# Kernel tuning notes

Hardware: AMD Instinct MI355X
Metric: run time of the kernel (lower is better)

The kernel has to match this reference:

```python
import jax, jax.numpy as jnp
import numpy as np

H = 128        # hidden_channels
R = 32         # num_rbf
L = 2          # num_layers
CUTOFF = 4.5   # cutoff_upper (cutoff_lower = 0)
N_ATOMS = 2048
N_EDGES = 32768


def _tensor_norm(t):
    # Frobenius norm squared over the trailing 3x3 -> [N, H]
    return jnp.sum(t * t, axis=(-2, -1))


def _decompose(t):
    # Split into isotropic (I), antisymmetric (A), traceless symmetric (S) parts.
    eye = jnp.eye(3, dtype=t.dtype)
    I = (jnp.trace(t, axis1=-2, axis2=-1) / 3.0)[..., None, None] * eye
    A = 0.5 * (t - jnp.swapaxes(t, -2, -1))
    S = 0.5 * (t + jnp.swapaxes(t, -2, -1)) - I
    return I, A, S


def _chan_mix(T, W):
    # torch nn.Linear(H, H, bias=False) applied on the channel axis of [N,H,3,3]
    return jnp.einsum('nhij,gh->ngij', T, W)


def _interaction(X, edge_index, edge_weight, edge_attr, q,
                 W1, b1, W2, b2, W3, b3, Wt):
    N = X.shape[0]
    src, dst = edge_index[0], edge_index[1]
    # cosine cutoff (cutoff_lower = 0)
    C = 0.5 * (jnp.cos(edge_weight * (jnp.pi / CUTOFF)) + 1.0)
    C = C * (edge_weight < CUTOFF).astype(C.dtype)
    # edge scalar MLP: R -> H -> 2H -> 3H, silu
    ea = jax.nn.silu(edge_attr @ W1.T + b1)
    ea = jax.nn.silu(ea @ W2.T + b2)
    ea = jax.nn.silu(ea @ W3.T + b3)
    ea = (ea * C[:, None]).reshape(-1, H, 3)       # [E, H, 3]
    # normalize node tensors
    X = X / (_tensor_norm(X) + 1.0)[..., None, None]
    I, A, S = _decompose(X)
    I = _chan_mix(I, Wt[0])
    A = _chan_mix(A, Wt[1])
    S = _chan_mix(S, Wt[2])
    Y = I + A + S
    # per-edge tensor messages (Im + Am + Sm fused before the scatter)
    msg = (ea[:, :, 0, None, None] * I[dst]
           + ea[:, :, 1, None, None] * A[dst]
           + ea[:, :, 2, None, None] * S[dst])   # [E, H, 3, 3]
    M = jax.ops.segment_sum(msg, src, num_segments=N)
    # O(3) group: symmetrized tensor product, scaled by charge factor
    AB = jnp.matmul(M, Y) + jnp.matmul(Y, M)
    I, A, S = _decompose((1.0 + 0.1 * q[:, None, None, None]) * AB)
    normp1 = (_tensor_norm(I + A + S) + 1.0)[..., None, None]
    I, A, S = I / normp1, A / normp1, S / normp1
    I = _chan_mix(I, Wt[3])
    A = _chan_mix(A, Wt[4])
    S = _chan_mix(S, Wt[5])
    dX = I + A + S
    return X + dX + (1.0 + 0.1 * q[:, None, None, None]) * jnp.matmul(dX, dX)


def setup_inputs() -> dict:
    key = jax.random.key(0)
    ks = jax.random.split(key, 10)
    N, E = N_ATOMS, N_EDGES
    X = jax.random.normal(ks[0], (N, H, 3, 3), jnp.float32)
    edge_index = jax.random.randint(ks[1], (2, E), 0, N, jnp.int32)
    edge_weight = jax.random.uniform(ks[2], (E,), jnp.float32, 0.1, CUTOFF)
    edge_attr = jax.random.normal(ks[3], (E, R), jnp.float32)
    q = jax.random.normal(ks[4], (N,), jnp.float32) * 0.1
    s = 0.05
    Ws1 = jax.random.normal(ks[5], (L, H, R), jnp.float32) * s
    bs1 = jnp.zeros((L, H), jnp.float32)
    Ws2 = jax.random.normal(ks[6], (L, 2 * H, H), jnp.float32) * s
    bs2 = jnp.zeros((L, 2 * H), jnp.float32)
    Ws3 = jax.random.normal(ks[7], (L, 3 * H, 2 * H), jnp.float32) * s
    bs3 = jnp.zeros((L, 3 * H), jnp.float32)
    Wt = jax.random.normal(ks[8], (L, 6, H, H), jnp.float32) * s
    return dict(X=X, edge_attr=edge_attr, edge_weight=edge_weight, q=q,
                Ws1=Ws1, bs1=bs1, Ws2=Ws2, bs2=bs2, Ws3=Ws3, bs3=bs3,
                Wt=Wt, edge_index=edge_index)


def reference(X, edge_attr, edge_weight, q, Ws1, bs1, Ws2, bs2, Ws3, bs3, Wt, edge_index):
    for l in range(L):
        X = _interaction(X, edge_index, edge_weight, edge_attr, q,
                         Ws1[l], bs1[l], Ws2[l], bs2[l], Ws3[l], bs3[l], Wt[l])
    return X
```

## Files before the change

kernel.cpp:

```cpp
#include <hip/hip_runtime.h>
#include <hip/hip_bf16.h>
#include <math.h>

#define H 128
#define R 32
#define NATOMS 2048
#define NEDGES 32768
#define NH (NATOMS * H)
#define NP 1152
#define CUTOFF_F 4.5f
#define PI_OVER_CUTOFF 0.6981317007977318f

typedef __bf16 bf16x8 __attribute__((ext_vector_type(8)));
typedef float f32x4 __attribute__((ext_vector_type(4)));
typedef short short8 __attribute__((ext_vector_type(8)));

__device__ __forceinline__ float silu_f(float x) {
    return x / (1.f + __expf(-x));
}
__device__ __forceinline__ float b2f(unsigned short u) {
    return __uint_as_float(((unsigned)u) << 16);
}
__device__ __forceinline__ unsigned short f2b(float f) {
    __hip_bfloat16 h = __float2bfloat16(f);
    return __builtin_bit_cast(unsigned short, h);
}

__device__ __forceinline__ void build_full(const float d[9], float m[9]) {
    float i0 = d[0], a01 = d[1], a02 = d[2], a12 = d[3];
    float s00 = d[4], s01 = d[5], s02 = d[6], s11 = d[7], s12 = d[8];
    float s22 = -(s00 + s11);
    m[0] = i0 + s00;  m[1] = a01 + s01;  m[2] = a02 + s02;
    m[3] = s01 - a01; m[4] = i0 + s11;   m[5] = a12 + s12;
    m[6] = s02 - a02; m[7] = s12 - a12;  m[8] = i0 + s22;
}

#define C0 (NEDGES * R)
#define C1 (2 * H * R)
#define C2 (2 * 2 * H * H)
#define C3 (2 * 3 * H * 2 * H)
#define C4 (2 * 6 * H * H)
#define CAST_TOTAL (C0 + C1 + C2 + C3 + C4 + 2048)
__global__ __launch_bounds__(256) void k_cast_all(
        const float* __restrict__ ea, const float* __restrict__ w1,
        const float* __restrict__ w2, const float* __restrict__ w3,
        const float* __restrict__ wt,
        __hip_bfloat16* __restrict__ oea, __hip_bfloat16* __restrict__ ow1,
        __hip_bfloat16* __restrict__ ow2, __hip_bfloat16* __restrict__ ow3,
        __hip_bfloat16* __restrict__ owt, int* __restrict__ cnt) {
    int i = blockIdx.x * 256 + threadIdx.x;
    if (i < C0) { oea[i] = __float2bfloat16(ea[i]); return; }
    i -= C0;
    if (i < C1) { ow1[i] = __float2bfloat16(w1[i]); return; }
    i -= C1;
    if (i < C2) { ow2[i] = __float2bfloat16(w2[i]); return; }
    i -= C2;
    if (i < C3) { ow3[i] = __float2bfloat16(w3[i]); return; }
    i -= C3;
    if (i < C4) { owt[i] = __float2bfloat16(wt[i]); return; }
    i -= C4;
    if (i < 2048) cnt[i] = 0;
}

__global__ __launch_bounds__(256) void k_node_prep(
        const float* __restrict__ X, float* __restrict__ Xn,
        __hip_bfloat16* __restrict__ Db) {
    int i = blockIdx.x * 256 + threadIdx.x;
    if (i >= NH) return;
    const float* x = X + (size_t)i * 9;
    float v[9];
    float ss = 0.f;
#pragma unroll
    for (int j = 0; j < 9; j++) { v[j] = x[j]; ss += v[j] * v[j]; }
    float inv = 1.f / (ss + 1.f);
#pragma unroll
    for (int j = 0; j < 9; j++) { v[j] *= inv; Xn[(size_t)i * 9 + j] = v[j]; }
    float i0 = (v[0] + v[4] + v[8]) * (1.f / 3.f);
    unsigned short* D = (unsigned short*)Db + (size_t)(i >> 7) * NP + (i & 127);
    D[0 * H] = f2b(i0);
    D[1 * H] = f2b(0.5f * (v[1] - v[3]));
    D[2 * H] = f2b(0.5f * (v[2] - v[6]));
    D[3 * H] = f2b(0.5f * (v[5] - v[7]));
    D[4 * H] = f2b(v[0] - i0);
    D[5 * H] = f2b(0.5f * (v[1] + v[3]));
    D[6 * H] = f2b(0.5f * (v[2] + v[6]));
    D[7 * H] = f2b(v[4] - i0);
    D[8 * H] = f2b(0.5f * (v[5] + v[7]));
}

struct TGm {
    static constexpr int BKm = 64;
    static constexpr int RB  = 128;
    static constexpr int SWZ = 7;
    static constexpr int NIT = 2;
    static constexpr int ABYTES = 128 * RB;
    static constexpr int BBYTES = 64 * RB;
    static constexpr int AISS = ABYTES / 4096;
    static constexpr int BISS = BBYTES / 4096;
    static constexpr int LDSB = ABYTES + BBYTES;
};

__device__ __forceinline__ void tile_gemm_mix(
        const __hip_bfloat16* __restrict__ A, int strideA,
        const __hip_bfloat16* __restrict__ W,
        int m0, int n0, char* lds, f32x4 acc[4][2]) {
    using T = TGm;
    const int t = threadIdx.x;
    const int lane = t & 63;
    const int w = t >> 6;

    auto stage = [&](int b, int it) {
        const int k0 = it * T::BKm;
        char* As = lds + b * T::LDSB;
        char* Bs = As + T::ABYTES;
#pragma unroll
        for (int i = 0; i < T::AISS; i++) {
            int base = (w * T::AISS + i) * 1024;
            int lin = base + lane * 16;
            int row = lin / T::RB;
            int slot = (lin % T::RB) >> 4;
            int sl = slot ^ (row & T::SWZ);
            const char* src = (const char*)(A + (size_t)(m0 + row) * strideA + k0) + sl * 16;
            __builtin_amdgcn_global_load_lds(
                (const __attribute__((address_space(1))) void*)src,
                (__attribute__((address_space(3))) void*)(As + base), 16, 0, 0);
        }
#pragma unroll
        for (int i = 0; i < T::BISS; i++) {
            int base = (w * T::BISS + i) * 1024;
            int lin = base + lane * 16;
            int row = lin / T::RB;
            int slot = (lin % T::RB) >> 4;
            int sl = slot ^ (row & T::SWZ);
            const char* src = (const char*)(W + (size_t)(n0 + row) * H + k0) + sl * 16;
            __builtin_amdgcn_global_load_lds(
                (const __attribute__((address_space(1))) void*)src,
                (__attribute__((address_space(3))) void*)(Bs + base), 16, 0, 0);
        }
    };

    auto compute = [&](int b) {
        const char* As = lds + b * T::LDSB;
        const char* Bs = As + T::ABYTES;
        const int wm = (w & 1) * 64;
        const int wn = (w >> 1) * 32;
        const int rA = wm + (lane & 15);
        const int rB = wn + (lane & 15);
        const int c = lane >> 4;
#pragma unroll
        for (int kk = 0; kk < T::BKm / 32; kk++) {
            bf16x8 av[4], bv[2];
#pragma unroll
            for (int mf = 0; mf < 4; mf++) {
                int row = rA + mf * 16;
                int sp = (kk * 4 + c) ^ (row & T::SWZ);
                av[mf] = __builtin_bit_cast(bf16x8,
                    *(const short8*)(As + row * T::RB + sp * 16));
            }
#pragma unroll
            for (int nf = 0; nf < 2; nf++) {
                int row = rB + nf * 16;
                int sp = (kk * 4 + c) ^ (row & T::SWZ);
                bv[nf] = __builtin_bit_cast(bf16x8,
                    *(const short8*)(Bs + row * T::RB + sp * 16));
            }
#pragma unroll
            for (int mf = 0; mf < 4; mf++)
#pragma unroll
                for (int nf = 0; nf < 2; nf++)
                    acc[mf][nf] = __builtin_amdgcn_mfma_f32_16x16x32_bf16(
                        av[mf], bv[nf], acc[mf][nf], 0, 0, 0);
        }
    };

    stage(0, 0);
    asm volatile("s_waitcnt vmcnt(0)" ::: "memory");
    __syncthreads();
    for (int it = 0; it < T::NIT; it++) {
        int b = it & 1;
        if (it + 1 < T::NIT) stage(b ^ 1, it + 1);
        compute(b);
        asm volatile("s_waitcnt vmcnt(0)" ::: "memory");
        __syncthreads();
    }
}

__global__ __launch_bounds__(256) void k_mix(
        const __hip_bfloat16* __restrict__ Db, const __hip_bfloat16* __restrict__ Wtb,
        __hip_bfloat16* __restrict__ Outp, int partOff) {
    __shared__ char lds[2 * TGm::LDSB];
    int c = blockIdx.z;
    int part = (c == 0) ? 0 : ((c < 4) ? 1 : 2);
    const __hip_bfloat16* A = Db + (size_t)c * H;
    const __hip_bfloat16* W = Wtb + (size_t)(partOff + part) * H * H;
    unsigned short* Out = (unsigned short*)Outp + (size_t)c * H;
    const int lane = threadIdx.x & 63;
    const int w = threadIdx.x >> 6;
    const int wm = (w & 1) * 64, wn = (w >> 1) * 32;
    const int m0 = blockIdx.x * 128, n0 = blockIdx.y * 64;
    f32x4 acc[4][2] = {};
    tile_gemm_mix(A, NP, W, m0, n0, lds, acc);
#pragma unroll
    for (int mf = 0; mf < 4; mf++)
#pragma unroll
        for (int r = 0; r < 4; r++) {
            int row = m0 + wm + mf * 16 + (lane >> 4) * 4 + r;
#pragma unroll
            for (int nf = 0; nf < 2; nf++) {
                int col = n0 + wn + nf * 16 + (lane & 15);
                Out[(size_t)row * NP + col] = f2b(acc[mf][nf][r]);
            }
        }
}

#define ETILE 64
#define PAD0 40
#define PAD1 136
#define PAD2 264
#define SA2_B (ETILE * PAD2 * 2)
#define SA1_B (ETILE * PAD1 * 2)
#define SEA_OFF SA1_B

__global__ __launch_bounds__(512, 4) void k_mlp_fused(
        const __hip_bfloat16* __restrict__ eaB,
        const __hip_bfloat16* __restrict__ W1b, const __hip_bfloat16* __restrict__ W2b,
        const __hip_bfloat16* __restrict__ W3b,
        const float* __restrict__ bs1, const float* __restrict__ bs2,
        const float* __restrict__ bs3, const float* __restrict__ ew,
        __hip_bfloat16* __restrict__ ea3g) {
    const int l = blockIdx.z;
    const unsigned short* W1 = (const unsigned short*)W1b + (size_t)l * (H * R);
    const unsigned short* W2 = (const unsigned short*)W2b + (size_t)l * (2 * H * H);
    const unsigned short* W3 = (const unsigned short*)W3b + (size_t)l * (3 * H * 2 * H);
    const float* b1 = bs1 + (size_t)l * H;
    const float* b2 = bs2 + (size_t)l * 2 * H;
    const float* b3 = bs3 + (size_t)l * 3 * H;
    unsigned short* outp = (unsigned short*)ea3g + (size_t)l * NEDGES * 384;
    const int e0 = blockIdx.x * ETILE;

    __shared__ char smem[SA2_B + ETILE * 4 + 16];
    unsigned short* sA2 = (unsigned short*)smem;
    unsigned short* sA1 = (unsigned short*)smem;
    unsigned short* sEA = (unsigned short*)(smem + SEA_OFF);
    float* sEW = (float*)(smem + SA2_B);

    const int t = threadIdx.x;
    const int lane = t & 63;
    const int w = t >> 6;
    const int q = lane >> 4;
    const int li = lane & 15;

    {
        if (t < 256) {
            int row = t >> 2, c8 = t & 3;
            *(uint4*)(sEA + row * PAD0 + c8 * 8) =
                *(const uint4*)((const unsigned short*)eaB + (size_t)(e0 + row) * R + c8 * 8);
        }
        if (t < ETILE) sEW[t] = ew[e0 + t];
    }
    __syncthreads();

    {
        f32x4 acc1[4] = {};
        const int col = w * 16 + li;
        bf16x8 bv = __builtin_bit_cast(bf16x8,
            *(const short8*)(W1 + (size_t)col * R + q * 8));
#pragma unroll
        for (int mf = 0; mf < 4; mf++) {
            int row = mf * 16 + li;
            bf16x8 av = __builtin_bit_cast(bf16x8,
                *(const short8*)(sEA + row * PAD0 + q * 8));
            acc1[mf] = __builtin_amdgcn_mfma_f32_16x16x32_bf16(
                av, bv, acc1[mf], 0, 0, 0);
        }
        float bb = b1[col];
#pragma unroll
        for (int mf = 0; mf < 4; mf++)
#pragma unroll
            for (int r = 0; r < 4; r++) {
                int row = mf * 16 + q * 4 + r;
                sA1[row * PAD1 + col] = f2b(silu_f(acc1[mf][r] + bb));
            }
    }
    __syncthreads();

    {
        f32x4 acc2[4][2] = {};
        bf16x8 b2v[2][2];
#pragma unroll
        for (int nf = 0; nf < 2; nf++)
            b2v[0][nf] = __builtin_bit_cast(bf16x8,
                *(const short8*)(W2 + (size_t)(w * 32 + nf * 16 + li) * H + q * 8));
#pragma unroll
        for (int ks = 0; ks < 4; ks++) {
            const int cur = ks & 1;
            if (ks < 3) {
#pragma unroll
                for (int nf = 0; nf < 2; nf++)
                    b2v[cur ^ 1][nf] = __builtin_bit_cast(bf16x8,
                        *(const short8*)(W2 + (size_t)(w * 32 + nf * 16 + li) * H
                                         + (ks + 1) * 32 + q * 8));
            }
            bf16x8 av[4];
#pragma unroll
            for (int mf = 0; mf < 4; mf++)
                av[mf] = __builtin_bit_cast(bf16x8,
                    *(const short8*)(sA1 + (mf * 16 + li) * PAD1 + ks * 32 + q * 8));
            __builtin_amdgcn_s_setprio(1);
#pragma unroll
            for (int mf = 0; mf < 4; mf++)
#pragma unroll
                for (int nf = 0; nf < 2; nf++)
                    acc2[mf][nf] = __builtin_amdgcn_mfma_f32_16x16x32_bf16(
                        av[mf], b2v[cur][nf], acc2[mf][nf], 0, 0, 0);
            __builtin_amdgcn_s_setprio(0);
        }
        float bb[2];
#pragma unroll
        for (int nf = 0; nf < 2; nf++) bb[nf] = b2[w * 32 + nf * 16 + li];
        __syncthreads();
#pragma unroll
        for (int mf = 0; mf < 4; mf++)
#pragma unroll
            for (int r = 0; r < 4; r++) {
                int row = mf * 16 + q * 4 + r;
#pragma unroll
                for (int nf = 0; nf < 2; nf++) {
                    int col = w * 32 + nf * 16 + li;
                    sA2[row * PAD2 + col] = f2b(silu_f(acc2[mf][nf][r] + bb[nf]));
                }
            }
    }
    __syncthreads();

#pragma unroll
    for (int hn = 0; hn < 2; hn++) {
        const int NF = (hn == 0) ? 2 : 1;
        const int cbase = w * 48 + hn * 32;
        f32x4 acc3[4][2] = {};
        bf16x8 b3v[2][2];
#pragma unroll
        for (int nf = 0; nf < 2; nf++)
            if (nf < NF)
                b3v[0][nf] = __builtin_bit_cast(bf16x8,
                    *(const short8*)(W3 + (size_t)(cbase + nf * 16 + li) * (2 * H) + q * 8));
#pragma unroll
        for (int ks = 0; ks < 8; ks++) {
            const int cur = ks & 1;
            if (ks < 7) {
#pragma unroll
                for (int nf = 0; nf < 2; nf++)
                    if (nf < NF)
                        b3v[cur ^ 1][nf] = __builtin_bit_cast(bf16x8,
                            *(const short8*)(W3 + (size_t)(cbase + nf * 16 + li) * (2 * H)
                                             + (ks + 1) * 32 + q * 8));
            }
            bf16x8 av[4];
#pragma unroll
            for (int mf = 0; mf < 4; mf++)
                av[mf] = __builtin_bit_cast(bf16x8,
                    *(const short8*)(sA2 + (mf * 16 + li) * PAD2 + ks * 32 + q * 8));
            __builtin_amdgcn_s_setprio(1);
#pragma unroll
            for (int mf = 0; mf < 4; mf++)
#pragma unroll
                for (int nf = 0; nf < 2; nf++)
                    if (nf < NF)
                        acc3[mf][nf] = __builtin_amdgcn_mfma_f32_16x16x32_bf16(
                            av[mf], b3v[cur][nf], acc3[mf][nf], 0, 0, 0);
            __builtin_amdgcn_s_setprio(0);
        }
        float bb[2];
#pragma unroll
        for (int nf = 0; nf < 2; nf++)
            bb[nf] = (nf < NF) ? b3[cbase + nf * 16 + li] : 0.f;
#pragma unroll
        for (int mf = 0; mf < 4; mf++)
#pragma unroll
            for (int r = 0; r < 4; r++) {
                int row = mf * 16 + q * 4 + r;
                float wv = sEW[row];
                float cs = (wv < CUTOFF_F) ? 0.5f * (__cosf(wv * PI_OVER_CUTOFF) + 1.f) : 0.f;
#pragma unroll
                for (int nf = 0; nf < 2; nf++)
                    if (nf < NF) {
                        int col = cbase + nf * 16 + li;
                        float x = silu_f(acc3[mf][nf][r] + bb[nf]) * cs;
                        outp[(size_t)(e0 + row) * 384 + col] = f2b(x);
                    }
            }
    }
}

__global__ __launch_bounds__(256) void k_hist(
        const int* __restrict__ eidx, int* __restrict__ cnt) {
    int e = blockIdx.x * 256 + threadIdx.x;
    if (e < NEDGES) atomicAdd(&cnt[eidx[e]], 1);
}

__global__ __launch_bounds__(256) void k_scan(
        const int* __restrict__ cnt, int* __restrict__ rowstart,
        int* __restrict__ cursor) {
    __shared__ int partial[256];
    int t = threadIdx.x;
    int loc[8];
    int run = 0;
#pragma unroll
    for (int j = 0; j < 8; j++) {
        int v = cnt[t * 8 + j];
        loc[j] = run; run += v;
    }
    partial[t] = run;
    __syncthreads();
    if (t == 0) {
        int acc = 0;
        for (int i = 0; i < 256; i++) { int v = partial[i]; partial[i] = acc; acc += v; }
        rowstart[2048] = acc;
    }
    __syncthreads();
    int base = partial[t];
#pragma unroll
    for (int j = 0; j < 8; j++) {
        rowstart[t * 8 + j] = base + loc[j];
        cursor[t * 8 + j] = base + loc[j];
    }
}

__global__ __launch_bounds__(256) void k_fill(
        const int* __restrict__ eidx, int* __restrict__ cursor,
        int* __restrict__ elist) {
    int e = blockIdx.x * 256 + threadIdx.x;
    if (e >= NEDGES) return;
    int src = eidx[e];
    int pos = atomicAdd(&cursor[src], 1);
    elist[pos] = e;
}

__global__ __launch_bounds__(256) void k_gather_ab(
        const __hip_bfloat16* __restrict__ ea ,
        const int* __restrict__ eidx,
        const int* __restrict__ rowstart, const int* __restrict__ elist,
        const __hip_bfloat16* __restrict__ Yb, const float* __restrict__ q,
        __hip_bfloat16* __restrict__ Tb) {
    int gid = blockIdx.x * 256 + threadIdx.x;
    int n = gid >> 7;
    int t7 = gid & 127;
    int hp = t7 >> 1;
    int half = t7 & 1;
    int h0 = hp << 1;
    int beg = rowstart[n], end = rowstart[n + 1];
    const unsigned short* Y = (const unsigned short*)Yb;
    float acc[9][2];
#pragma unroll
    for (int c = 0; c < 9; c++) { acc[c][0] = 0.f; acc[c][1] = 0.f; }
    for (int idx = beg + half; idx < end; idx += 2) {
        int e = elist[idx];
        int dst = eidx[NEDGES + e];
        const unsigned short* eap = (const unsigned short*)ea + (size_t)e * 384 + h0 * 3;
        unsigned u0 = *(const unsigned*)(eap);
        unsigned u1 = *(const unsigned*)(eap + 2);
        unsigned u2 = *(const unsigned*)(eap + 4);
        float w0a = b2f(u0 & 0xffff), w1a = b2f(u0 >> 16);
        float w2a = b2f(u1 & 0xffff), w0b = b2f(u1 >> 16);
        float w1b = b2f(u2 & 0xffff), w2b = b2f(u2 >> 16);
        const unsigned short* yp = Y + (size_t)dst * NP + h0;
        ushort2 y;
        y = *(const ushort2*)(yp + 0 * H); acc[0][0] += w0a * b2f(y.x); acc[0][1] += w0b * b2f(y.y);
        y = *(const ushort2*)(yp + 1 * H); acc[1][0] += w1a * b2f(y.x); acc[1][1] += w1b * b2f(y.y);
        y = *(const ushort2*)(yp + 2 * H); acc[2][0] += w1a * b2f(y.x); acc[2][1] += w1b * b2f(y.y);
        y = *(const ushort2*)(yp + 3 * H); acc[3][0] += w1a * b2f(y.x); acc[3][1] += w1b * b2f(y.y);
#pragma unroll
        for (int c = 4; c < 9; c++) {
            y = *(const ushort2*)(yp + c * H);
            acc[c][0] += w2a * b2f(y.x); acc[c][1] += w2b * b2f(y.y);
        }
    }
#pragma unroll
    for (int c = 0; c < 9; c++) {
        acc[c][0] += __shfl_xor(acc[c][0], 1);
        acc[c][1] += __shfl_xor(acc[c][1], 1);
    }
    int hcol = h0 + half;
    const unsigned short* yp = Y + (size_t)n * NP + hcol;
    float scale = 1.f + 0.1f * q[n];
    float md[9], yd[9];
#pragma unroll
    for (int c = 0; c < 9; c++) {
        md[c] = acc[c][half];
        yd[c] = b2f(yp[(size_t)c * H]);
    }
    float m[9], yf[9];
    build_full(md, m);
    build_full(yd, yf);
    float ab[9];
#pragma unroll
    for (int ii = 0; ii < 3; ii++)
#pragma unroll
        for (int jj = 0; jj < 3; jj++) {
            float s = 0.f;
#pragma unroll
            for (int kk = 0; kk < 3; kk++)
                s += m[ii * 3 + kk] * yf[kk * 3 + jj] + yf[ii * 3 + kk] * m[kk * 3 + jj];
            ab[ii * 3 + jj] = s;
        }
    float nrm = 0.f;
#pragma unroll
    for (int j = 0; j < 9; j++) { ab[j] *= scale; nrm += ab[j] * ab[j]; }
    float inv = 1.f / (nrm + 1.f);
    float tr3 = (ab[0] + ab[4] + ab[8]) * (1.f / 3.f);
    unsigned short* T = (unsigned short*)Tb + (size_t)n * NP + hcol;
    T[0 * H] = f2b(tr3 * inv);
    T[1 * H] = f2b(0.5f * (ab[1] - ab[3]) * inv);
    T[2 * H] = f2b(0.5f * (ab[2] - ab[6]) * inv);
    T[3 * H] = f2b(0.5f * (ab[5] - ab[7]) * inv);
    T[4 * H] = f2b((ab[0] - tr3) * inv);
    T[5 * H] = f2b(0.5f * (ab[1] + ab[3]) * inv);
    T[6 * H] = f2b(0.5f * (ab[2] + ab[6]) * inv);
    T[7 * H] = f2b((ab[4] - tr3) * inv);
    T[8 * H] = f2b(0.5f * (ab[5] + ab[7]) * inv);
}

template <bool PREP>
__global__ __launch_bounds__(256) void k_final(
        const __hip_bfloat16* __restrict__ dXb, const float* __restrict__ Xn,
        const float* __restrict__ q, float* __restrict__ Xout,
        float* __restrict__ XnW, __hip_bfloat16* __restrict__ Db) {
    int i = blockIdx.x * 256 + threadIdx.x;
    if (i >= NH) return;
    const unsigned short* dX = (const unsigned short*)dXb + (size_t)(i >> 7) * NP + (i & 127);
    float dd[9];
#pragma unroll
    for (int c = 0; c < 9; c++) dd[c] = b2f(dX[(size_t)c * H]);
    float dx[9];
    build_full(dd, dx);
    float scale = 1.f + 0.1f * q[i >> 7];
    float out[9];
#pragma unroll
    for (int ii = 0; ii < 3; ii++)
#pragma unroll
        for (int jj = 0; jj < 3; jj++) {
            float s = 0.f;
#pragma unroll
            for (int kk = 0; kk < 3; kk++)
                s += dx[ii * 3 + kk] * dx[kk * 3 + jj];
            out[ii * 3 + jj] = Xn[(size_t)i * 9 + ii * 3 + jj] + dx[ii * 3 + jj] + scale * s;
        }
#pragma unroll
    for (int j = 0; j < 9; j++) Xout[(size_t)i * 9 + j] = out[j];
    if (PREP) {
        float ss = 0.f;
#pragma unroll
        for (int j = 0; j < 9; j++) ss += out[j] * out[j];
        float inv = 1.f / (ss + 1.f);
        float v[9];
#pragma unroll
        for (int j = 0; j < 9; j++) { v[j] = out[j] * inv; XnW[(size_t)i * 9 + j] = v[j]; }
        float i0 = (v[0] + v[4] + v[8]) * (1.f / 3.f);
        unsigned short* D = (unsigned short*)Db + (size_t)(i >> 7) * NP + (i & 127);
        D[0 * H] = f2b(i0);
        D[1 * H] = f2b(0.5f * (v[1] - v[3]));
        D[2 * H] = f2b(0.5f * (v[2] - v[6]));
        D[3 * H] = f2b(0.5f * (v[5] - v[7]));
        D[4 * H] = f2b(v[0] - i0);
        D[5 * H] = f2b(0.5f * (v[1] + v[3]));
        D[6 * H] = f2b(0.5f * (v[2] + v[6]));
        D[7 * H] = f2b(v[4] - i0);
        D[8 * H] = f2b(0.5f * (v[5] + v[7]));
    }
}

extern "C" void kernel_launch(void* const* d_in, const int* in_sizes, int n_in,
                              void* d_out, int out_size, void* d_ws, size_t ws_size,
                              hipStream_t stream) {
    const float* X          = (const float*)d_in[0];
    const float* edge_attr  = (const float*)d_in[1];
    const float* edge_weight= (const float*)d_in[2];
    const float* q          = (const float*)d_in[3];
    const float* Ws1        = (const float*)d_in[4];
    const float* bs1        = (const float*)d_in[5];
    const float* Ws2        = (const float*)d_in[6];
    const float* bs2        = (const float*)d_in[7];
    const float* Ws3        = (const float*)d_in[8];
    const float* bs3        = (const float*)d_in[9];
    const float* Wt         = (const float*)d_in[10];
    const int*   eidx       = (const int*)d_in[11];
    float* Xout = (float*)d_out;

    char* p = (char*)d_ws;
    auto alloc = [&](size_t bytes) -> char* {
        char* r = p; p += (bytes + 255) & ~(size_t)255; return r;
    };
    size_t nodeBytes = (size_t)NH * 9 * sizeof(float);
    float* Xn   = (float*)alloc(nodeBytes);
    __hip_bfloat16* Db = (__hip_bfloat16*)alloc((size_t)NH * 9 * 2);
    __hip_bfloat16* Yb = (__hip_bfloat16*)alloc((size_t)NH * 9 * 2);
    __hip_bfloat16* eaB = (__hip_bfloat16*)alloc((size_t)C0 * 2);
    __hip_bfloat16* W1b = (__hip_bfloat16*)alloc((size_t)C1 * 2);
    __hip_bfloat16* W2b = (__hip_bfloat16*)alloc((size_t)C2 * 2);
    __hip_bfloat16* W3b = (__hip_bfloat16*)alloc((size_t)C3 * 2);
    __hip_bfloat16* Wtb = (__hip_bfloat16*)alloc((size_t)C4 * 2);
    __hip_bfloat16* ea3g = (__hip_bfloat16*)alloc((size_t)2 * NEDGES * 384 * 2);
    int* cnt      = (int*)alloc(2048 * 4);
    int* rowstart = (int*)alloc(2049 * 4);
    int* cursor   = (int*)alloc(2048 * 4);
    int* elist    = (int*)alloc(NEDGES * 4);

    k_cast_all<<<(CAST_TOTAL + 255) / 256, 256, 0, stream>>>(
        edge_attr, Ws1, Ws2, Ws3, Wt, eaB, W1b, W2b, W3b, Wtb, cnt);

    k_hist<<<NEDGES / 256, 256, 0, stream>>>(eidx, cnt);
    k_scan<<<1, 256, 0, stream>>>(cnt, rowstart, cursor);
    k_fill<<<NEDGES / 256, 256, 0, stream>>>(eidx, cursor, elist);

    k_node_prep<<<NH / 256, 256, 0, stream>>>(X, Xn, Db);

    k_mlp_fused<<<dim3(NEDGES / ETILE, 1, 2), 512, 0, stream>>>(
        eaB, W1b, W2b, W3b, bs1, bs2, bs3, edge_weight, ea3g);

    for (int l = 0; l < 2; l++) {
        const __hip_bfloat16* Wtl = Wtb + (size_t)l * 6 * H * H;
        const __hip_bfloat16* ea3 = ea3g + (size_t)l * NEDGES * 384;

        k_mix<<<dim3(NATOMS / 128, 2, 9), 256, 0, stream>>>(Db, Wtl, Yb, 0);
        k_gather_ab<<<NH / 256, 256, 0, stream>>>(
            ea3, eidx, rowstart, elist, Yb, q, Db);
        k_mix<<<dim3(NATOMS / 128, 2, 9), 256, 0, stream>>>(Db, Wtl, Yb, 3);
        if (l == 0)
            k_final<true><<<NH / 256, 256, 0, stream>>>(Yb, Xn, q, Xout, Xn, Db);
        else
            k_final<false><<<NH / 256, 256, 0, stream>>>(Yb, Xn, q, Xout, nullptr, nullptr);
    }
}
```

Baseline: 161.5 us.

## Transpose edge-MLP MFMA operands for vectorized stores and fold node prep into cast

The edge MLP GEMMs swap operand roles so weights become the A operand and edge activations the B operand. Each lane then holds four consecutive output channels and can write them as one 8-byte vector to LDS and global memory instead of scalar bf16 stores. The third layer is also restructured from two column halves into a single 3x4 fragment pass, and biases are loaded as float4. Separately, the node normalization and decomposition is merged into the cast kernel to remove one launch, at the cost of more registers in the third GEMM and a larger combined kernel.

Result: no change. 163.5 us (+1.3%).

```diff
diff --git a/kernel.cpp b/kernel.cpp
--- a/kernel.cpp
+++ b/kernel.cpp
@@ -14,6 +14,7 @@
 typedef __bf16 bf16x8 __attribute__((ext_vector_type(8)));
 typedef float f32x4 __attribute__((ext_vector_type(4)));
 typedef short short8 __attribute__((ext_vector_type(8)));
+typedef unsigned short u16x4 __attribute__((ext_vector_type(4)));
 
 __device__ __forceinline__ float silu_f(float x) {
     return x / (1.f + __expf(-x));
@@ -40,14 +41,17 @@
 #define C2 (2 * 2 * H * H)
 #define C3 (2 * 3 * H * 2 * H)
 #define C4 (2 * 6 * H * H)
-#define CAST_TOTAL (C0 + C1 + C2 + C3 + C4 + 2048)
+#define C5 2048
+#define CAST_TOTAL (C0 + C1 + C2 + C3 + C4 + C5 + NH)
 __global__ __launch_bounds__(256) void k_cast_all(
         const float* __restrict__ ea, const float* __restrict__ w1,
         const float* __restrict__ w2, const float* __restrict__ w3,
         const float* __restrict__ wt,
         __hip_bfloat16* __restrict__ oea, __hip_bfloat16* __restrict__ ow1,
         __hip_bfloat16* __restrict__ ow2, __hip_bfloat16* __restrict__ ow3,
-        __hip_bfloat16* __restrict__ owt, int* __restrict__ cnt) {
+        __hip_bfloat16* __restrict__ owt, int* __restrict__ cnt,
+        const float* __restrict__ X, float* __restrict__ Xn,
+        __hip_bfloat16* __restrict__ Db) {
     int i = blockIdx.x * 256 + threadIdx.x;
     if (i < C0) { oea[i] = __float2bfloat16(ea[i]); return; }
     i -= C0;
@@ -59,33 +63,29 @@
     i -= C3;
     if (i < C4) { owt[i] = __float2bfloat16(wt[i]); return; }
     i -= C4;
-    if (i < 2048) cnt[i] = 0;
-}
-
-__global__ __launch_bounds__(256) void k_node_prep(
-        const float* __restrict__ X, float* __restrict__ Xn,
-        __hip_bfloat16* __restrict__ Db) {
-    int i = blockIdx.x * 256 + threadIdx.x;
-    if (i >= NH) return;
-    const float* x = X + (size_t)i * 9;
-    float v[9];
-    float ss = 0.f;
-#pragma unroll
-    for (int j = 0; j < 9; j++) { v[j] = x[j]; ss += v[j] * v[j]; }
-    float inv = 1.f / (ss + 1.f);
-#pragma unroll
-    for (int j = 0; j < 9; j++) { v[j] *= inv; Xn[(size_t)i * 9 + j] = v[j]; }
-    float i0 = (v[0] + v[4] + v[8]) * (1.f / 3.f);
-    unsigned short* D = (unsigned short*)Db + (size_t)(i >> 7) * NP + (i & 127);
-    D[0 * H] = f2b(i0);
-    D[1 * H] = f2b(0.5f * (v[1] - v[3]));
-    D[2 * H] = f2b(0.5f * (v[2] - v[6]));
-    D[3 * H] = f2b(0.5f * (v[5] - v[7]));
-    D[4 * H] = f2b(v[0] - i0);
-    D[5 * H] = f2b(0.5f * (v[1] + v[3]));
-    D[6 * H] = f2b(0.5f * (v[2] + v[6]));
-    D[7 * H] = f2b(v[4] - i0);
-    D[8 * H] = f2b(0.5f * (v[5] + v[7]));
+    if (i < C5) { cnt[i] = 0; return; }
+    i -= C5;
+    if (i < NH) {
+        const float* x = X + (size_t)i * 9;
+        float v[9];
+        float ss = 0.f;
+#pragma unroll
+        for (int j = 0; j < 9; j++) { v[j] = x[j]; ss += v[j] * v[j]; }
+        float inv = 1.f / (ss + 1.f);
+#pragma unroll
+        for (int j = 0; j < 9; j++) { v[j] *= inv; Xn[(size_t)i * 9 + j] = v[j]; }
+        float i0 = (v[0] + v[4] + v[8]) * (1.f / 3.f);
+        unsigned short* D = (unsigned short*)Db + (size_t)(i >> 7) * NP + (i & 127);
+        D[0 * H] = f2b(i0);
+        D[1 * H] = f2b(0.5f * (v[1] - v[3]));
+        D[2 * H] = f2b(0.5f * (v[2] - v[6]));
+        D[3 * H] = f2b(0.5f * (v[5] - v[7]));
+        D[4 * H] = f2b(v[0] - i0);
+        D[5 * H] = f2b(0.5f * (v[1] + v[3]));
+        D[6 * H] = f2b(0.5f * (v[2] + v[6]));
+        D[7 * H] = f2b(v[4] - i0);
+        D[8 * H] = f2b(0.5f * (v[5] + v[7]));
+    }
 }
 
 struct TGm {
@@ -261,134 +261,127 @@
     __syncthreads();
 
     {
+        const int cbase1 = w * 16;
         f32x4 acc1[4] = {};
-        const int col = w * 16 + li;
-        bf16x8 bv = __builtin_bit_cast(bf16x8,
-            *(const short8*)(W1 + (size_t)col * R + q * 8));
-#pragma unroll
-        for (int mf = 0; mf < 4; mf++) {
-            int row = mf * 16 + li;
-            bf16x8 av = __builtin_bit_cast(bf16x8,
-                *(const short8*)(sEA + row * PAD0 + q * 8));
-            acc1[mf] = __builtin_amdgcn_mfma_f32_16x16x32_bf16(
-                av, bv, acc1[mf], 0, 0, 0);
-        }
-        float bb = b1[col];
-#pragma unroll
-        for (int mf = 0; mf < 4; mf++)
-#pragma unroll
-            for (int r = 0; r < 4; r++) {
-                int row = mf * 16 + q * 4 + r;
-                sA1[row * PAD1 + col] = f2b(silu_f(acc1[mf][r] + bb));
-            }
+        bf16x8 av = __builtin_bit_cast(bf16x8,
+            *(const short8*)(W1 + (size_t)(cbase1 + li) * R + q * 8));
+#pragma unroll
+        for (int ef = 0; ef < 4; ef++) {
+            bf16x8 bv = __builtin_bit_cast(bf16x8,
+                *(const short8*)(sEA + (ef * 16 + li) * PAD0 + q * 8));
+            acc1[ef] = __builtin_amdgcn_mfma_f32_16x16x32_bf16(av, bv, acc1[ef], 0, 0, 0);
+        }
+        f32x4 bb = *(const f32x4*)&b1[cbase1 + q * 4];
+#pragma unroll
+        for (int ef = 0; ef < 4; ef++) {
+            u16x4 o;
+#pragma unroll
+            for (int r = 0; r < 4; r++) o[r] = f2b(silu_f(acc1[ef][r] + bb[r]));
+            *(u16x4*)(sA1 + (ef * 16 + li) * PAD1 + cbase1 + q * 4) = o;
+        }
     }
     __syncthreads();
 
     {
-        f32x4 acc2[4][2] = {};
-        bf16x8 b2v[2][2];
-#pragma unroll
-        for (int nf = 0; nf < 2; nf++)
-            b2v[0][nf] = __builtin_bit_cast(bf16x8,
-                *(const short8*)(W2 + (size_t)(w * 32 + nf * 16 + li) * H + q * 8));
+        const int cbase2 = w * 32;
+        f32x4 acc2[2][4] = {};
+        bf16x8 a2[2][2];
+#pragma unroll
+        for (int mf = 0; mf < 2; mf++)
+            a2[0][mf] = __builtin_bit_cast(bf16x8,
+                *(const short8*)(W2 + (size_t)(cbase2 + mf * 16 + li) * H + q * 8));
 #pragma unroll
         for (int ks = 0; ks < 4; ks++) {
             const int cur = ks & 1;
             if (ks < 3) {
 #pragma unroll
-                for (int nf = 0; nf < 2; nf++)
-                    b2v[cur ^ 1][nf] = __builtin_bit_cast(bf16x8,
-                        *(const short8*)(W2 + (size_t)(w * 32 + nf * 16 + li) * H
+                for (int mf = 0; mf < 2; mf++)
+                    a2[cur ^ 1][mf] = __builtin_bit_cast(bf16x8,
+                        *(const short8*)(W2 + (size_t)(cbase2 + mf * 16 + li) * H
                                          + (ks + 1) * 32 + q * 8));
             }
-            bf16x8 av[4];
-#pragma unroll
-            for (int mf = 0; mf < 4; mf++)
-                av[mf] = __builtin_bit_cast(bf16x8,
-                    *(const short8*)(sA1 + (mf * 16 + li) * PAD1 + ks * 32 + q * 8));
+            bf16x8 bv[4];
+#pragma unroll
+            for (int ef = 0; ef < 4; ef++)
+                bv[ef] = __builtin_bit_cast(bf16x8,
+                    *(const short8*)(sA1 + (ef * 16 + li) * PAD1 + ks * 32 + q * 8));
             __builtin_amdgcn_s_setprio(1);
 #pragma unroll
-            for (int mf = 0; mf < 4; mf++)
-#pragma unroll
-                for (int nf = 0; nf < 2; nf++)
-                    acc2[mf][nf] = __builtin_amdgcn_mfma_f32_16x16x32_bf16(
-                        av[mf], b2v[cur][nf], acc2[mf][nf], 0, 0, 0);
+            for (int mf = 0; mf < 2; mf++)
+#pragma unroll
+                for (int ef = 0; ef < 4; ef++)
+                    acc2[mf][ef] = __builtin_amdgcn_mfma_f32_16x16x32_bf16(
+                        a2[cur][mf], bv[ef], acc2[mf][ef], 0, 0, 0);
             __builtin_amdgcn_s_setprio(0);
         }
-        float bb[2];
-#pragma unroll
-        for (int nf = 0; nf < 2; nf++) bb[nf] = b2[w * 32 + nf * 16 + li];
+        f32x4 bb[2];
+#pragma unroll
+        for (int mf = 0; mf < 2; mf++)
+            bb[mf] = *(const f32x4*)&b2[cbase2 + mf * 16 + q * 4];
         __syncthreads();
 #pragma unroll
-        for (int mf = 0; mf < 4; mf++)
-#pragma unroll
-            for (int r = 0; r < 4; r++) {
-                int row = mf * 16 + q * 4 + r;
-#pragma unroll
-                for (int nf = 0; nf < 2; nf++) {
-                    int col = w * 32 + nf * 16 + li;
-                    sA2[row * PAD2 + col] = f2b(silu_f(acc2[mf][nf][r] + bb[nf]));
-                }
+        for (int mf = 0; mf < 2; mf++)
+#pragma unroll
+            for (int ef = 0; ef < 4; ef++) {
+                u16x4 o;
+#pragma unroll
+                for (int r = 0; r < 4; r++)
+                    o[r] = f2b(silu_f(acc2[mf][ef][r] + bb[mf][r]));
+                *(u16x4*)(sA2 + (ef * 16 + li) * PAD2 + cbase2 + mf * 16 + q * 4) = o;
             }
     }
     __syncthreads();
 
-#pragma unroll
-    for (int hn = 0; hn < 2; hn++) {
-        const int NF = (hn == 0) ? 2 : 1;
-        const int cbase = w * 48 + hn * 32;
-        f32x4 acc3[4][2] = {};
-        bf16x8 b3v[2][2];
-#pragma unroll
-        for (int nf = 0; nf < 2; nf++)
-            if (nf < NF)
-                b3v[0][nf] = __builtin_bit_cast(bf16x8,
-                    *(const short8*)(W3 + (size_t)(cbase + nf * 16 + li) * (2 * H) + q * 8));
+    {
+        const int cbase3 = w * 48;
+        f32x4 acc3[3][4] = {};
+        bf16x8 a3[2][3];
+#pragma unroll
+        for (int mf = 0; mf < 3; mf++)
+            a3[0][mf] = __builtin_bit_cast(bf16x8,
+                *(const short8*)(W3 + (size_t)(cbase3 + mf * 16 + li) * (2 * H) + q * 8));
 #pragma unroll
         for (int ks = 0; ks < 8; ks++) {
             const int cur = ks & 1;
             if (ks < 7) {
 #pragma unroll
-                for (int nf = 0; nf < 2; nf++)
-                    if (nf < NF)
-                        b3v[cur ^ 1][nf] = __builtin_bit_cast(bf16x8,
-                            *(const short8*)(W3 + (size_t)(cbase + nf * 16 + li) * (2 * H)
-                                             + (ks + 1) * 32 + q * 8));
+                for (int mf = 0; mf < 3; mf++)
+                    a3[cur ^ 1][mf] = __builtin_bit_cast(bf16x8,
+                        *(const short8*)(W3 + (size_t)(cbase3 + mf * 16 + li) * (2 * H)
+                                         + (ks + 1) * 32 + q * 8));
             }
-            bf16x8 av[4];
-#pragma unroll
-            for (int mf = 0; mf < 4; mf++)
-                av[mf] = __builtin_bit_cast(bf16x8,
-                    *(const short8*)(sA2 + (mf * 16 + li) * PAD2 + ks * 32 + q * 8));
+            bf16x8 bv[4];
+#pragma unroll
+            for (int ef = 0; ef < 4; ef++)
+                bv[ef] = __builtin_bit_cast(bf16x8,
+                    *(const short8*)(sA2 + (ef * 16 + li) * PAD2 + ks * 32 + q * 8));
             __builtin_amdgcn_s_setprio(1);
 #pragma unroll
-            for (int mf = 0; mf < 4; mf++)
-#pragma unroll
-                for (int nf = 0; nf < 2; nf++)
-                    if (nf < NF)
-                        acc3[mf][nf] = __builtin_amdgcn_mfma_f32_16x16x32_bf16(
-                            av[mf], b3v[cur][nf], acc3[mf][nf], 0, 0, 0);
+            for (int mf = 0; mf < 3; mf++)
+#pragma unroll
+                for (int ef = 0; ef < 4; ef++)
+                    acc3[mf][ef] = __builtin_amdgcn_mfma_f32_16x16x32_bf16(
+                        a3[cur][mf], bv[ef], acc3[mf][ef], 0, 0, 0);
             __builtin_amdgcn_s_setprio(0);
         }
-        float bb[2];
-#pragma unroll
-        for (int nf = 0; nf < 2; nf++)
-            bb[nf] = (nf < NF) ? b3[cbase + nf * 16 + li] : 0.f;
-#pragma unroll
-        for (int mf = 0; mf < 4; mf++)
-#pragma unroll
-            for (int r = 0; r < 4; r++) {
-                int row = mf * 16 + q * 4 + r;
-                float wv = sEW[row];
-                float cs = (wv < CUTOFF_F) ? 0.5f * (__cosf(wv * PI_OVER_CUTOFF) + 1.f) : 0.f;
-#pragma unroll
-                for (int nf = 0; nf < 2; nf++)
-                    if (nf < NF) {
-                        int col = cbase + nf * 16 + li;
-                        float x = silu_f(acc3[mf][nf][r] + bb[nf]) * cs;
-                        outp[(size_t)(e0 + row) * 384 + col] = f2b(x);
-                    }
+        f32x4 bb[3];
+#pragma unroll
+        for (int mf = 0; mf < 3; mf++)
+            bb[mf] = *(const f32x4*)&b3[cbase3 + mf * 16 + q * 4];
+#pragma unroll
+        for (int ef = 0; ef < 4; ef++) {
+            int edge = ef * 16 + li;
+            float wv = sEW[edge];
+            float cs = (wv < CUTOFF_F) ? 0.5f * (__cosf(wv * PI_OVER_CUTOFF) + 1.f) : 0.f;
+#pragma unroll
+            for (int mf = 0; mf < 3; mf++) {
+                u16x4 o;
+#pragma unroll
+                for (int r = 0; r < 4; r++)
+                    o[r] = f2b(silu_f(acc3[mf][ef][r] + bb[mf][r]) * cs);
+                *(u16x4*)(outp + (size_t)(e0 + edge) * 384 + cbase3 + mf * 16 + q * 4) = o;
             }
+        }
     }
 }
 
@@ -606,13 +599,12 @@
     int* elist    = (int*)alloc(NEDGES * 4);
 
     k_cast_all<<<(CAST_TOTAL + 255) / 256, 256, 0, stream>>>(
-        edge_attr, Ws1, Ws2, Ws3, Wt, eaB, W1b, W2b, W3b, Wtb, cnt);
+        edge_attr, Ws1, Ws2, Ws3, Wt, eaB, W1b, W2b, W3b, Wtb, cnt,
+        X, Xn, Db);
 
     k_hist<<<NEDGES / 256, 256, 0, stream>>>(eidx, cnt);
     k_scan<<<1, 256, 0, stream>>>(cnt, rowstart, cursor);
     k_fill<<<NEDGES / 256, 256, 0, stream>>>(eidx, cursor, elist);
-
-    k_node_prep<<<NH / 256, 256, 0, stream>>>(X, Xn, Db);
 
     k_mlp_fused<<<dim3(NEDGES / ETILE, 1, 2), 512, 0, stream>>>(
         eaB, W1b, W2b, W3b, bs1, bs2, bs3, edge_weight, ea3g);
```
